# Optimization experiments

Hardware: AMD Instinct MI355X
Metric: run time of the kernel (lower is better)

Reference implementation:

```python
import jax, jax.numpy as jnp
import numpy as np

B, S, H, I, E, TOP_K = 1, 2048, 1024, 4096, 8, 1


def setup_inputs() -> dict:
    key = jax.random.key(0)
    ks = jax.random.split(key, 8)
    s = 0.02  # init scale for weights
    return {
        "hidden_states": jax.random.normal(ks[0], (B, S, H), jnp.float32),
        "router_w": jax.random.normal(ks[1], (E, H), jnp.float32) * s,
        "w_gate": jax.random.normal(ks[2], (E, I, H), jnp.float32) * s,
        "w_up": jax.random.normal(ks[3], (E, I, H), jnp.float32) * s,
        "w_down": jax.random.normal(ks[4], (E, H, I), jnp.float32) * s,
        "ws_gate": jax.random.normal(ks[5], (I, H), jnp.float32) * s,
        "ws_up": jax.random.normal(ks[6], (I, H), jnp.float32) * s,
        "ws_down": jax.random.normal(ks[7], (H, I), jnp.float32) * s,
    }


def _mlp(x, wg, wu, wd):
    # silu(x @ Wg^T) * (x @ Wu^T) @ Wd^T  (Llama4TextMLP)
    return (jax.nn.silu(x @ wg.T) * (x @ wu.T)) @ wd.T


def reference(hidden_states, router_w, w_gate, w_up, w_down, ws_gate, ws_up, ws_down):
    b, s, h = hidden_states.shape
    hs = hidden_states.reshape(-1, h)                      # [T, H]
    T = hs.shape[0]
    logits = hs @ router_w.T                               # [T, E]
    top_v, top_i = jax.lax.top_k(logits, TOP_K)            # [T, K]
    masked = jnp.full_like(logits, -jnp.inf)
    masked = masked.at[jnp.arange(T)[:, None], top_i].set(top_v)
    scores = jax.nn.sigmoid(masked)                        # [T, E]; sigmoid(-inf)=0

    # In this module every expert sees ALL tokens, scaled by its (mostly-zero) score.
    routed = scores.T[:, :, None] * hs[None, :, :]         # [E, T, H]

    out = _mlp(hs, ws_gate, ws_up, ws_down)                # shared expert, [T, H]
    gate = jnp.einsum('eth,eih->eti', routed, w_gate)      # [E, T, I]
    up = jnp.einsum('eth,eih->eti', routed, w_up)          # [E, T, I]
    expert_out = jnp.einsum('eti,ehi->eth', jax.nn.silu(gate) * up, w_down)
    out = out + expert_out.sum(axis=0)                     # [T, H]
    return out, scores.T                                   # router_scores is [E, T]
```

## Files before the change

kernel.cpp:

```cpp
#include <hip/hip_runtime.h>
#include <hip/hip_bf16.h>
#include <math.h>

#define T_TOK 2048
#define HDIM 1024
#define IDIM 4096
#define NEXP 8
#define RROWS 3200
#define AROWS 5248
#define ZROW  5120
#define NP2   24
#define BK 32

typedef unsigned int uint;
typedef unsigned short ushort;
typedef __attribute__((ext_vector_type(4))) float f32x4;
typedef __attribute__((ext_vector_type(8))) short bf16x8;

__device__ __forceinline__ ushort f2bf(float f) {
  union { float f; uint u; } c; c.f = f;
  uint u = c.u;
  return (ushort)((u + 0x7FFFu + ((u >> 16) & 1u)) >> 16);
}
__device__ __forceinline__ uint cvtpk(float a, float b) {
  uint r;
  asm("v_cvt_pk_bf16_f32 %0, %1, %2" : "=v"(r) : "v"(a), "v"(b));
  return r;
}
__device__ __forceinline__ void gld16(ushort* lds, const ushort* g) {
  __builtin_amdgcn_global_load_lds(
      (const __attribute__((address_space(1))) uint*)g,
      (__attribute__((address_space(3))) uint*)lds, 16, 0, 0);
}
__device__ __forceinline__ int soff(int row, int kc) {
  return ((row >> 4) << 9) + (kc << 7) + ((row & 15) << 3);
}

#define SYNCV(N) { \
  __builtin_amdgcn_sched_barrier(0); \
  asm volatile("s_waitcnt vmcnt(" #N ") lgkmcnt(0)" ::: "memory"); \
  __builtin_amdgcn_s_barrier(); \
  __builtin_amdgcn_sched_barrier(0); }

__global__ __launch_bounds__(256) void router_kernel(
    const float* __restrict__ hs, const float* __restrict__ rw,
    ushort* __restrict__ Xall, float* __restrict__ scores_out,
    int* __restrict__ eidx, float* __restrict__ sval)
{
  const int wave = threadIdx.x >> 6;
  const int lane = threadIdx.x & 63;
  const int t = blockIdx.x * 4 + wave;
  const float* row = hs + (size_t)t * HDIM;
  float v[16];
  #pragma unroll
  for (int i = 0; i < 16; ++i) {
    v[i] = row[lane + 64 * i];
    Xall[(size_t)t * HDIM + lane + 64 * i] = f2bf(v[i]);
  }
  float logit[8];
  #pragma unroll
  for (int e = 0; e < 8; ++e) {
    const float* wr = rw + e * HDIM;
    float s = 0.f;
    #pragma unroll
    for (int i = 0; i < 16; ++i) s += v[i] * wr[lane + 64 * i];
    #pragma unroll
    for (int off = 32; off; off >>= 1) s += __shfl_xor(s, off, 64);
    logit[e] = s;
  }
  if (lane == 0) {
    int be = 0; float bv = logit[0];
    #pragma unroll
    for (int e = 1; e < 8; ++e) if (logit[e] > bv) { bv = logit[e]; be = e; }
    float sc = 1.f / (1.f + expf(-bv));
    eidx[t] = be; sval[t] = sc;
    #pragma unroll
    for (int e = 0; e < 8; ++e) scores_out[(size_t)e * T_TOK + t] = (e == be) ? sc : 0.f;
  }
}

__global__ __launch_bounds__(256) void plan_kernel(
    const int* __restrict__ eidx, int* __restrict__ row2tok, int4* __restrict__ pairs)
{
  __shared__ int cnt[8];
  __shared__ int slot[8];
  const int tid = threadIdx.x;
  if (tid < 8) cnt[tid] = 0;
  __syncthreads();
  for (int t = tid; t < T_TOK; t += 256) atomicAdd(&cnt[eidx[t]], 1);
  __syncthreads();
  if (tid == 0) {
    int np = 0;
    for (int i = 0; i < 8; ++i) pairs[np++] = make_int4(i * 256, i * 256 + 128, -1, 1);
    int o = 0;
    for (int e = 0; e < 8; ++e) {
      slot[e] = o;
      int cap = (cnt[e] + 127) & ~127;
      int nt = cap / 128;
      for (int j = 0; j < nt; j += 2) {
        int ra = T_TOK + o + j * 128;
        int rb = (j + 1 < nt) ? ra + 128 : ZROW;
        pairs[np++] = make_int4(ra, rb, e, 1);
      }
      o += cap;
    }
    for (; np < NP2; ++np) pairs[np] = make_int4(ZROW, ZROW, 0, 0);
  }
  for (int r = tid; r < RROWS; r += 256) row2tok[r] = -1;
  __syncthreads();
  for (int t = tid; t < T_TOK; t += 256) {
    int e = eidx[t];
    int s = atomicAdd(&slot[e], 1);
    row2tok[s] = t;
  }
}

__global__ __launch_bounds__(256) void gather_kernel(
    const float* __restrict__ hs, const int* __restrict__ row2tok,
    const float* __restrict__ sval, ushort* __restrict__ Xall)
{
  const int r = blockIdx.x;
  const int t = row2tok[r];
  const int c0 = threadIdx.x * 4;
  ushort4 o;
  if (t >= 0) {
    const float sc = sval[t];
    float4 v = *(const float4*)(hs + (size_t)t * HDIM + c0);
    o.x = f2bf(sc * v.x); o.y = f2bf(sc * v.y); o.z = f2bf(sc * v.z); o.w = f2bf(sc * v.w);
  } else { o.x = o.y = o.z = o.w = 0; }
  *(ushort4*)(Xall + (size_t)(T_TOK + r) * HDIM + c0) = o;
}

#define LOADB1(S, k0) { \
  gr##S = *(const float4*)(gptr + (k0)); \
  ur##S = *(const float4*)(uptr + (k0)); }

#define WRITEB1(S, B) { \
  *(uint2*)&Bg[B][woff] = make_uint2(cvtpk(gr##S.x, gr##S.y), cvtpk(gr##S.z, gr##S.w)); \
  *(uint2*)&Bu[B][woff] = make_uint2(cvtpk(ur##S.x, ur##S.y), cvtpk(ur##S.z, ur##S.w)); }

#define STAGEA(ABASE, k0) { gld16((ABASE) + alds0, asrc0 + (k0)); }

#define READ1(ABASE, B) \
  bf16x8 af[4], gf[2], uf[2]; \
  _Pragma("unroll") \
  for (int m = 0; m < 4; ++m) af[m] = *(const bf16x8*)((ABASE) + (wm*4+m)*512 + lp); \
  _Pragma("unroll") \
  for (int n = 0; n < 2; ++n) { \
    gf[n] = *(const bf16x8*)&Bg[B][(wn*2+n)*512 + lp]; \
    uf[n] = *(const bf16x8*)&Bu[B][(wn*2+n)*512 + lp]; }

#define MFMA1 \
  _Pragma("unroll") \
  for (int m = 0; m < 4; ++m) { \
    _Pragma("unroll") \
    for (int n = 0; n < 2; ++n) { \
      accg[m][n] = __builtin_amdgcn_mfma_f32_16x16x32_bf16(af[m], gf[n], accg[m][n], 0, 0, 0); \
      accu[m][n] = __builtin_amdgcn_mfma_f32_16x16x32_bf16(af[m], uf[n], accu[m][n], 0, 0, 0); } }

#define ROTA { ushort* aT_ = aR; aR = aM; aM = aS; aS = aT_; }

__global__ __launch_bounds__(1024, 1) void gemm1_kernel(
    const ushort* __restrict__ Xall,
    const float* __restrict__ w_gate, const float* __restrict__ w_up,
    const float* __restrict__ ws_gate, const float* __restrict__ ws_up,
    const int4* __restrict__ pairs, ushort* __restrict__ actall)
{
  __shared__ __align__(16) ushort As[3][8192];
  __shared__ __align__(16) ushort Bg[2][4096];
  __shared__ __align__(16) ushort Bu[2][4096];

  const int b0 = blockIdx.x;
  const int j = b0 & 7, s = b0 >> 3;
  const int panel = j + 8 * (s / NP2);
  const int4 td = pairs[s % NP2];
  if (td.w == 0) return;
  const int r0a = td.x, r0b = td.y, e = td.z;
  const float* __restrict__ gbase = (e < 0) ? ws_gate : w_gate + (size_t)e * IDIM * HDIM;
  const float* __restrict__ ubase = (e < 0) ? ws_up   : w_up   + (size_t)e * IDIM * HDIM;
  const int col0 = panel * 128;

  const int tid = threadIdx.x;
  const int lane = tid & 63;
  const int w = tid >> 6;
  const int wm = w >> 2, wn = w & 3;

  const int brow = tid >> 3, bch = tid & 7;
  const float* gptr = gbase + (size_t)(col0 + brow) * HDIM + bch * 4;
  const float* uptr = ubase + (size_t)(col0 + brow) * HDIM + bch * 4;
  const int woff = soff(brow, bch >> 1) + (bch & 1) * 4;

  const size_t abs0 = (w < 8) ? (size_t)(r0a + w * 16 + (lane & 15))
                              : (size_t)(r0b + (w - 8) * 16 + (lane & 15));
  const ushort* asrc0 = Xall + abs0 * HDIM + (lane >> 4) * 8;
  const int alds0 = w * 512 + lane * 8;

  ushort* aR = &As[0][0];
  ushort* aM = &As[1][0];
  ushort* aS = &As[2][0];

  float4 gr0, ur0, gr1, ur1;
  const int lp = (lane >> 4) * 128 + (lane & 15) * 8;
  f32x4 accg[4][2] = {};
  f32x4 accu[4][2] = {};

  STAGEA(aR, 0);
  LOADB1(0, 0);
  STAGEA(aM, BK);
  LOADB1(1, BK);
  WRITEB1(0, 0);
  SYNCV(3);

  const int NS = HDIM / BK;
  for (int kk = 0; kk < NS / 2 - 1; ++kk) {
    const int k = kk * 2;
    {
      READ1(aR, 0);
      STAGEA(aS, (k + 2) * BK);
      LOADB1(0, (k + 2) * BK);
      MFMA1;
      WRITEB1(1, 1);
      SYNCV(3);
      ROTA;
    }
    {
      READ1(aR, 1);
      STAGEA(aS, (k + 3) * BK);
      LOADB1(1, (k + 3) * BK);
      MFMA1;
      WRITEB1(0, 0);
      SYNCV(3);
      ROTA;
    }
  }
  {
    READ1(aR, 0);
    MFMA1;
    WRITEB1(1, 1);
    SYNCV(0);
    ROTA;
  }
  {
    READ1(aR, 1);
    MFMA1;
  }

  const int prbase = wm * 64 + ((lane >> 4) << 2);
  const int cbase = col0 + wn * 32 + (lane & 15);
  #pragma unroll
  for (int m = 0; m < 4; ++m)
    #pragma unroll
    for (int n = 0; n < 2; ++n)
      #pragma unroll
      for (int j2 = 0; j2 < 4; ++j2) {
        const int pr = prbase + m * 16 + j2;
        const size_t ar = (wm < 2) ? (size_t)(r0a + pr) : (size_t)(r0b + pr - 128);
        float g = accg[m][n][j2];
        float u = accu[m][n][j2];
        float sv = g / (1.f + __expf(-g)) * u;
        actall[ar * IDIM + cbase + n * 16] = f2bf(sv);
      }
}

#define LOADB2(S, k0) { br##S = *(const float4*)(bptr + (k0)); }

#define WRITEB2(S, B) { \
  *(uint2*)&Bs[B][woff] = make_uint2(cvtpk(br##S.x, br##S.y), cvtpk(br##S.z, br##S.w)); }

#define READ2(ABASE, B) \
  bf16x8 af[4], bfr[2]; \
  _Pragma("unroll") \
  for (int m = 0; m < 4; ++m) af[m] = *(const bf16x8*)((ABASE) + (wm*4+m)*512 + lp); \
  _Pragma("unroll") \
  for (int n = 0; n < 2; ++n) bfr[n] = *(const bf16x8*)&Bs[B][(wn*2+n)*512 + lp];

#define MFMA2 \
  _Pragma("unroll") \
  for (int m = 0; m < 4; ++m) { \
    _Pragma("unroll") \
    for (int n = 0; n < 2; ++n) \
      acc[m][n] = __builtin_amdgcn_mfma_f32_16x16x32_bf16(af[m], bfr[n], acc[m][n], 0, 0, 0); }

__global__ __launch_bounds__(1024, 1) void gemm2_kernel(
    const ushort* __restrict__ actall,
    const float* __restrict__ w_down, const float* __restrict__ ws_down,
    const int4* __restrict__ pairs, const int* __restrict__ row2tok,
    float* __restrict__ out, float* __restrict__ bufr)
{
  __shared__ __align__(16) ushort As[3][8192];
  __shared__ __align__(16) ushort Bs[2][4096];

  const int b0 = blockIdx.x;
  const int panel = b0 & 7;
  const int4 td = pairs[b0 >> 3];
  if (td.w == 0) return;
  const int r0a = td.x, r0b = td.y, e = td.z;
  const float* __restrict__ bbase = (e < 0) ? ws_down : w_down + (size_t)e * HDIM * IDIM;
  const int col0 = panel * 128;

  const int tid = threadIdx.x;
  const int lane = tid & 63;
  const int w = tid >> 6;
  const int wm = w >> 2, wn = w & 3;

  const int brow = tid >> 3, bch = tid & 7;
  const float* bptr = bbase + (size_t)(col0 + brow) * IDIM + bch * 4;
  const int woff = soff(brow, bch >> 1) + (bch & 1) * 4;

  const size_t abs0 = (w < 8) ? (size_t)(r0a + w * 16 + (lane & 15))
                              : (size_t)(r0b + (w - 8) * 16 + (lane & 15));
  const ushort* asrc0 = actall + abs0 * IDIM + (lane >> 4) * 8;
  const int alds0 = w * 512 + lane * 8;

  ushort* aR = &As[0][0];
  ushort* aM = &As[1][0];
  ushort* aS = &As[2][0];

  float4 br0, br1;
  const int lp = (lane >> 4) * 128 + (lane & 15) * 8;
  f32x4 acc[4][2] = {};

  STAGEA(aR, 0);
  LOADB2(0, 0);
  STAGEA(aM, BK);
  LOADB2(1, BK);
  WRITEB2(0, 0);
  SYNCV(2);

  const int NS = IDIM / BK;
  for (int kk = 0; kk < NS / 2 - 1; ++kk) {
    const int k = kk * 2;
    {
      READ2(aR, 0);
      STAGEA(aS, (k + 2) * BK);
      LOADB2(0, (k + 2) * BK);
      MFMA2;
      WRITEB2(1, 1);
      SYNCV(2);
      ROTA;
    }
    {
      READ2(aR, 1);
      STAGEA(aS, (k + 3) * BK);
      LOADB2(1, (k + 3) * BK);
      MFMA2;
      WRITEB2(0, 0);
      SYNCV(2);
      ROTA;
    }
  }
  {
    READ2(aR, 0);
    MFMA2;
    WRITEB2(1, 1);
    SYNCV(0);
    ROTA;
  }
  {
    READ2(aR, 1);
    MFMA2;
  }

  const int prbase = wm * 64 + ((lane >> 4) << 2);
  const int cbase = col0 + wn * 32 + (lane & 15);
  #pragma unroll
  for (int m = 0; m < 4; ++m)
    #pragma unroll
    for (int j2 = 0; j2 < 4; ++j2) {
      const int pr = prbase + m * 16 + j2;
      const int ar = (wm < 2) ? (r0a + pr) : (r0b + pr - 128);
      if (e < 0) {
        #pragma unroll
        for (int n = 0; n < 2; ++n)
          out[(size_t)ar * HDIM + cbase + n * 16] = acc[m][n][j2];
      } else {
        const int t = row2tok[ar - T_TOK];
        if (t >= 0) {
          #pragma unroll
          for (int n = 0; n < 2; ++n)
            bufr[(size_t)t * HDIM + cbase + n * 16] = acc[m][n][j2];
        }
      }
    }
}

__global__ __launch_bounds__(256) void add_kernel(
    float* __restrict__ out, const float* __restrict__ bufr)
{
  const size_t i = ((size_t)blockIdx.x * 256 + threadIdx.x) * 4;
  float4 a = *(float4*)(out + i);
  const float4 b = *(const float4*)(bufr + i);
  a.x += b.x; a.y += b.y; a.z += b.z; a.w += b.w;
  *(float4*)(out + i) = a;
}

extern "C" void kernel_launch(void* const* d_in, const int* in_sizes, int n_in,
                              void* d_out, int out_size, void* d_ws, size_t ws_size,
                              hipStream_t stream)
{
  const float* hs      = (const float*)d_in[0];
  const float* rw      = (const float*)d_in[1];
  const float* w_gate  = (const float*)d_in[2];
  const float* w_up    = (const float*)d_in[3];
  const float* w_down  = (const float*)d_in[4];
  const float* ws_gate = (const float*)d_in[5];
  const float* ws_up   = (const float*)d_in[6];
  const float* ws_down = (const float*)d_in[7];

  float* out = (float*)d_out;
  float* scores_out = out + (size_t)T_TOK * HDIM;

  char* ws = (char*)d_ws;
  ushort* Xall   = (ushort*)ws;
  ushort* actall = (ushort*)(ws + 10747904);
  float*  bufr   = (float*)(ws + 53739520);
  int*    eidx   = (int*)(ws + 62128128);
  float*  sval   = (float*)(ws + 62136320);
  int*    r2t    = (int*)(ws + 62144512);
  int4*   pairs  = (int4*)(ws + 62157312);

  router_kernel<<<T_TOK / 4, 256, 0, stream>>>(hs, rw, Xall, scores_out, eidx, sval);
  plan_kernel<<<1, 256, 0, stream>>>(eidx, r2t, pairs);
  gather_kernel<<<RROWS, 256, 0, stream>>>(hs, r2t, sval, Xall);
  gemm1_kernel<<<(IDIM / 128) * NP2, 1024, 0, stream>>>(
      Xall, w_gate, w_up, ws_gate, ws_up, pairs, actall);
  gemm2_kernel<<<(HDIM / 128) * NP2, 1024, 0, stream>>>(
      actall, w_down, ws_down, pairs, r2t, out, bufr);
  add_kernel<<<(T_TOK * HDIM) / 1024, 256, 0, stream>>>(out, bufr);
}
```

Measured before the change: 308.6 us.

## Halve gemm2 block to 8 waves with 64x64 per-wave tiles; move B writes before MFMA

gemm2 now runs 512 threads instead of 1024. Each wave computes a 64x64 output tile (4x4 MFMA fragments) instead of 64x32, and each thread loads 8 floats of the B weights and two A rows per stage, writing a 16-byte packed bf16 vector. In both GEMMs, the LDS write of the next B tile is moved ahead of the MFMA block so the conversion and store can overlap with the matrix ops. The goal is more register reuse per LDS read and fewer waves contending for barriers, at the cost of higher register pressure and less latency hiding from wave count.

```diff
diff --git a/kernel.cpp b/kernel.cpp
--- a/kernel.cpp
+++ b/kernel.cpp
@@ -25,6 +25,12 @@
 __device__ __forceinline__ uint cvtpk(float a, float b) {
   uint r;
   asm("v_cvt_pk_bf16_f32 %0, %1, %2" : "=v"(r) : "v"(a), "v"(b));
+  return r;
+}
+__device__ __forceinline__ uint4 cvt8(const float4 a, const float4 b) {
+  uint4 r;
+  r.x = cvtpk(a.x, a.y); r.y = cvtpk(a.z, a.w);
+  r.z = cvtpk(b.x, b.y); r.w = cvtpk(b.z, b.w);
   return r;
 }
 __device__ __forceinline__ void gld16(ushort* lds, const ushort* g) {
@@ -139,7 +145,7 @@
   *(uint2*)&Bg[B][woff] = make_uint2(cvtpk(gr##S.x, gr##S.y), cvtpk(gr##S.z, gr##S.w)); \
   *(uint2*)&Bu[B][woff] = make_uint2(cvtpk(ur##S.x, ur##S.y), cvtpk(ur##S.z, ur##S.w)); }
 
-#define STAGEA(ABASE, k0) { gld16((ABASE) + alds0, asrc0 + (k0)); }
+#define STAGEA1(ABASE, k0) { gld16((ABASE) + alds0, asrc0 + (k0)); }
 
 #define READ1(ABASE, B) \
   bf16x8 af[4], gf[2], uf[2]; \
@@ -204,9 +210,9 @@
   f32x4 accg[4][2] = {};
   f32x4 accu[4][2] = {};
 
-  STAGEA(aR, 0);
+  STAGEA1(aR, 0);
   LOADB1(0, 0);
-  STAGEA(aM, BK);
+  STAGEA1(aM, BK);
   LOADB1(1, BK);
   WRITEB1(0, 0);
   SYNCV(3);
@@ -216,27 +222,27 @@
     const int k = kk * 2;
     {
       READ1(aR, 0);
-      STAGEA(aS, (k + 2) * BK);
+      STAGEA1(aS, (k + 2) * BK);
       LOADB1(0, (k + 2) * BK);
+      WRITEB1(1, 1);
       MFMA1;
-      WRITEB1(1, 1);
       SYNCV(3);
       ROTA;
     }
     {
       READ1(aR, 1);
-      STAGEA(aS, (k + 3) * BK);
+      STAGEA1(aS, (k + 3) * BK);
       LOADB1(1, (k + 3) * BK);
+      WRITEB1(0, 0);
       MFMA1;
-      WRITEB1(0, 0);
       SYNCV(3);
       ROTA;
     }
   }
   {
     READ1(aR, 0);
+    WRITEB1(1, 1);
     MFMA1;
-    WRITEB1(1, 1);
     SYNCV(0);
     ROTA;
   }
@@ -262,26 +268,31 @@
       }
 }
 
-#define LOADB2(S, k0) { br##S = *(const float4*)(bptr + (k0)); }
-
-#define WRITEB2(S, B) { \
-  *(uint2*)&Bs[B][woff] = make_uint2(cvtpk(br##S.x, br##S.y), cvtpk(br##S.z, br##S.w)); }
+#define LOADB2(S, k0) { \
+  const float4* bp_ = (const float4*)(bptr + (k0)); \
+  br##S[0] = bp_[0]; br##S[1] = bp_[1]; }
+
+#define WRITEB2(S, B) { *(uint4*)&Bs[B][woff2] = cvt8(br##S[0], br##S[1]); }
+
+#define STAGEA2(ABASE, k0) { \
+  gld16((ABASE) + alds0, asrc0 + (k0)); \
+  gld16((ABASE) + alds1, asrc1 + (k0)); }
 
 #define READ2(ABASE, B) \
-  bf16x8 af[4], bfr[2]; \
+  bf16x8 af[4], bfr[4]; \
   _Pragma("unroll") \
   for (int m = 0; m < 4; ++m) af[m] = *(const bf16x8*)((ABASE) + (wm*4+m)*512 + lp); \
   _Pragma("unroll") \
-  for (int n = 0; n < 2; ++n) bfr[n] = *(const bf16x8*)&Bs[B][(wn*2+n)*512 + lp];
+  for (int n = 0; n < 4; ++n) bfr[n] = *(const bf16x8*)&Bs[B][(wn*4+n)*512 + lp];
 
 #define MFMA2 \
   _Pragma("unroll") \
   for (int m = 0; m < 4; ++m) { \
     _Pragma("unroll") \
-    for (int n = 0; n < 2; ++n) \
+    for (int n = 0; n < 4; ++n) \
       acc[m][n] = __builtin_amdgcn_mfma_f32_16x16x32_bf16(af[m], bfr[n], acc[m][n], 0, 0, 0); }
 
-__global__ __launch_bounds__(1024, 1) void gemm2_kernel(
+__global__ __launch_bounds__(512, 1) void gemm2_kernel(
     const ushort* __restrict__ actall,
     const float* __restrict__ w_down, const float* __restrict__ ws_down,
     const int4* __restrict__ pairs, const int* __restrict__ row2tok,
@@ -301,58 +312,60 @@
   const int tid = threadIdx.x;
   const int lane = tid & 63;
   const int w = tid >> 6;
-  const int wm = w >> 2, wn = w & 3;
-
-  const int brow = tid >> 3, bch = tid & 7;
-  const float* bptr = bbase + (size_t)(col0 + brow) * IDIM + bch * 4;
-  const int woff = soff(brow, bch >> 1) + (bch & 1) * 4;
-
-  const size_t abs0 = (w < 8) ? (size_t)(r0a + w * 16 + (lane & 15))
-                              : (size_t)(r0b + (w - 8) * 16 + (lane & 15));
+  const int wm = w >> 1, wn = w & 1;
+
+  const int brow = tid >> 2, kcb = tid & 3;
+  const float* bptr = bbase + (size_t)(col0 + brow) * IDIM + kcb * 8;
+  const int woff2 = soff(brow, kcb);
+
+  const int arow = w * 32 + (lane & 15);
+  const size_t abs0 = (w < 4) ? (size_t)(r0a + arow) : (size_t)(r0b + arow - 128);
   const ushort* asrc0 = actall + abs0 * IDIM + (lane >> 4) * 8;
-  const int alds0 = w * 512 + lane * 8;
+  const ushort* asrc1 = asrc0 + (size_t)16 * IDIM;
+  const int alds0 = w * 1024 + lane * 8;
+  const int alds1 = alds0 + 512;
 
   ushort* aR = &As[0][0];
   ushort* aM = &As[1][0];
   ushort* aS = &As[2][0];
 
-  float4 br0, br1;
+  float4 br0[2], br1[2];
   const int lp = (lane >> 4) * 128 + (lane & 15) * 8;
-  f32x4 acc[4][2] = {};
-
-  STAGEA(aR, 0);
+  f32x4 acc[4][4] = {};
+
+  STAGEA2(aR, 0);
   LOADB2(0, 0);
-  STAGEA(aM, BK);
+  STAGEA2(aM, BK);
   LOADB2(1, BK);
   WRITEB2(0, 0);
-  SYNCV(2);
+  SYNCV(4);
 
   const int NS = IDIM / BK;
   for (int kk = 0; kk < NS / 2 - 1; ++kk) {
     const int k = kk * 2;
     {
       READ2(aR, 0);
-      STAGEA(aS, (k + 2) * BK);
+      STAGEA2(aS, (k + 2) * BK);
       LOADB2(0, (k + 2) * BK);
+      WRITEB2(1, 1);
       MFMA2;
-      WRITEB2(1, 1);
-      SYNCV(2);
+      SYNCV(4);
       ROTA;
     }
     {
       READ2(aR, 1);
-      STAGEA(aS, (k + 3) * BK);
+      STAGEA2(aS, (k + 3) * BK);
       LOADB2(1, (k + 3) * BK);
+      WRITEB2(0, 0);
       MFMA2;
-      WRITEB2(0, 0);
-      SYNCV(2);
+      SYNCV(4);
       ROTA;
     }
   }
   {
     READ2(aR, 0);
+    WRITEB2(1, 1);
     MFMA2;
-    WRITEB2(1, 1);
     SYNCV(0);
     ROTA;
   }
@@ -362,7 +375,7 @@
   }
 
   const int prbase = wm * 64 + ((lane >> 4) << 2);
-  const int cbase = col0 + wn * 32 + (lane & 15);
+  const int cbase = col0 + wn * 64 + (lane & 15);
   #pragma unroll
   for (int m = 0; m < 4; ++m)
     #pragma unroll
@@ -371,13 +384,13 @@
       const int ar = (wm < 2) ? (r0a + pr) : (r0b + pr - 128);
       if (e < 0) {
         #pragma unroll
-        for (int n = 0; n < 2; ++n)
+        for (int n = 0; n < 4; ++n)
           out[(size_t)ar * HDIM + cbase + n * 16] = acc[m][n][j2];
       } else {
         const int t = row2tok[ar - T_TOK];
         if (t >= 0) {
           #pragma unroll
-          for (int n = 0; n < 2; ++n)
+          for (int n = 0; n < 4; ++n)
             bufr[(size_t)t * HDIM + cbase + n * 16] = acc[m][n][j2];
         }
       }
@@ -424,7 +437,7 @@
   gather_kernel<<<RROWS, 256, 0, stream>>>(hs, r2t, sval, Xall);
   gemm1_kernel<<<(IDIM / 128) * NP2, 1024, 0, stream>>>(
       Xall, w_gate, w_up, ws_gate, ws_up, pairs, actall);
-  gemm2_kernel<<<(HDIM / 128) * NP2, 1024, 0, stream>>>(
+  gemm2_kernel<<<(HDIM / 128) * NP2, 512, 0, stream>>>(
       actall, w_down, ws_down, pairs, r2t, out, bufr);
   add_kernel<<<(T_TOK * HDIM) / 1024, 256, 0, stream>>>(out, bufr);
 }
```

Result: slower. 329.4 us (+6.8%).
